# Optimization experiments

Measured on AMD Instinct MI355X. Metric: run time of the kernel, lower is better.

Reference implementation:

```python
import jax, jax.numpy as jnp
import numpy as np

DIM = 128
EPS = 1e-5

def _layernorm(x, w, b, eps=EPS):
    mu = jnp.mean(x, axis=-1, keepdims=True)
    var = jnp.mean(jnp.square(x - mu), axis=-1, keepdims=True)
    return (x - mu) * jax.lax.rsqrt(var + eps) * w + b

def setup_inputs() -> dict:
    key = jax.random.key(0)
    ks = jax.random.split(key, 6)
    B, N, D = 1, 512, DIM
    x = jax.random.normal(ks[0], (B, N, N, D), dtype=jnp.float32)
    mask = jnp.ones((B, N, N), dtype=jnp.float32)
    # parameters (torch Linear weight is [out, in]; we store [in, out] for x @ W)
    lecun = 1.0 / np.sqrt(D)
    w_p_in = jax.random.normal(ks[1], (D, 2 * D), dtype=jnp.float32) * lecun
    w_g_in = jnp.zeros((D, 2 * D), dtype=jnp.float32)   # gating_init -> zeros
    w_p_out = jnp.zeros((D, D), dtype=jnp.float32)      # final_init -> zeros
    w_g_out = jnp.zeros((D, D), dtype=jnp.float32)      # gating_init -> zeros
    # use small random values instead of exact zeros to make the math non-trivial
    w_g_in = jax.random.normal(ks[2], (D, 2 * D), dtype=jnp.float32) * 0.02
    w_p_out = jax.random.normal(ks[3], (D, D), dtype=jnp.float32) * 0.02
    w_g_out = jax.random.normal(ks[4], (D, D), dtype=jnp.float32) * 0.02
    norm_in_w = jnp.ones((D,), jnp.float32)
    norm_in_b = jnp.zeros((D,), jnp.float32)
    norm_out_w = jnp.ones((D,), jnp.float32)
    norm_out_b = jnp.zeros((D,), jnp.float32)
    return {
        "x": x, "mask": mask,
        "w_p_in": w_p_in, "w_g_in": w_g_in,
        "w_p_out": w_p_out, "w_g_out": w_g_out,
        "norm_in_w": norm_in_w, "norm_in_b": norm_in_b,
        "norm_out_w": norm_out_w, "norm_out_b": norm_out_b,
    }

def reference(x, mask, w_p_in, w_g_in, w_p_out, w_g_out,
              norm_in_w, norm_in_b, norm_out_w, norm_out_b):
    # x: [B,N,N,D], mask: [B,N,N]
    xn = _layernorm(x, norm_in_w, norm_in_b)          # norm_in
    x_in = xn
    p = xn @ w_p_in                                   # [B,N,N,2D]
    g = jax.nn.sigmoid(xn @ w_g_in)
    h = p * g * mask[..., None]                       # gated + masked
    a, b = jnp.split(h.astype(jnp.float32), 2, axis=-1)  # each [B,N,N,D]
    t = jnp.einsum('bikd,bjkd->bijd', a, b)           # triangular matmul
    tn = _layernorm(t, norm_out_w, norm_out_b)        # norm_out (eps=1e-5)
    out = (tn @ w_p_out) * jax.nn.sigmoid(x_in @ w_g_out)
    return out
```

## Files before the change

### kernel.cpp

```cpp
#include <hip/hip_runtime.h>
#include <hip/hip_bf16.h>
#include <math.h>

#define NN 512
#define DD 128
#define NP (NN*NN)

#define PITCH ((size_t)(NP * 2 + 256))

typedef __attribute__((ext_vector_type(4))) float f32x4;
typedef __attribute__((ext_vector_type(8))) short bf16x8;

__device__ __forceinline__ unsigned short f2bf(float f) {
  union { float f; unsigned u; } v; v.f = f;
  unsigned r = v.u + 0x7FFFu + ((v.u >> 16) & 1u);
  return (unsigned short)(r >> 16);
}
__device__ __forceinline__ float bf2f(unsigned short h) {
  union { unsigned u; float f; } v; v.u = ((unsigned)h) << 16;
  return v.f;
}
__device__ __forceinline__ float sigmoidf_(float x) {
  return __builtin_amdgcn_rcpf(1.0f + __expf(-x));
}
__device__ __forceinline__ unsigned pkbf2(float a, float b) {
  float2 t; t.x = a; t.y = b;
  __hip_bfloat162 h = __float22bfloat162_rn(t);
  unsigned r; __builtin_memcpy(&r, &h, 4); return r;
}

__device__ __forceinline__ void gll16(void* lds, const void* g) {
  __builtin_amdgcn_global_load_lds(
      (const __attribute__((address_space(1))) void*)g,
      (__attribute__((address_space(3))) void*)lds, 16, 0, 0);
}

#define WP_P  0
#define WP_G  65536
#define WP_GO 131072
#define WP_PO 163840

__global__ __launch_bounds__(256) void kw_prep(const float* __restrict__ w_p_in,
    const float* __restrict__ w_g_in, const float* __restrict__ w_g_out,
    const float* __restrict__ w_p_out, unsigned short* __restrict__ wprep) {
  int idx = blockIdx.x * 256 + threadIdx.x;
  int n, k, base; float v;
  if (idx < 32768)       { n = idx >> 7;          k = idx & 127; v = w_p_in[k * 256 + n];  base = WP_P; }
  else if (idx < 65536)  { int e = idx - 32768;  n = e >> 7; k = e & 127; v = w_g_in[k * 256 + n];  base = WP_G; }
  else if (idx < 81920)  { int e = idx - 65536;  n = e >> 7; k = e & 127; v = w_g_out[k * 128 + n]; base = WP_GO; }
  else                   { int e = idx - 81920;  n = e >> 7; k = e & 127; v = w_p_out[k * 128 + n]; base = WP_PO; }
  int dst = base + n * 256 + ((2 * k) ^ ((n & 7) << 4));
  wprep[dst >> 1] = f2bf(v);
}

__global__ __launch_bounds__(256) void kA_ln(const float* __restrict__ x,
    const float* __restrict__ nw, const float* __restrict__ nb,
    unsigned short* __restrict__ xn_sw) {
  const int tid = threadIdx.x;
  const int l16 = tid & 15, rsub = tid >> 4;
  const int row0 = blockIdx.x * 64;
  const float4 wv0 = *(const float4*)(nw + l16 * 8);
  const float4 wv1 = *(const float4*)(nw + l16 * 8 + 4);
  const float4 bv0 = *(const float4*)(nb + l16 * 8);
  const float4 bv1 = *(const float4*)(nb + l16 * 8 + 4);
  #pragma unroll
  for (int rnd = 0; rnd < 4; ++rnd) {
    int r = row0 + rnd * 16 + rsub;
    const float* xr = x + (size_t)r * DD + l16 * 8;
    float4 v0 = *(const float4*)xr;
    float4 v1 = *(const float4*)(xr + 4);
    float s = v0.x + v0.y + v0.z + v0.w + v1.x + v1.y + v1.z + v1.w;
    float q = v0.x*v0.x + v0.y*v0.y + v0.z*v0.z + v0.w*v0.w
            + v1.x*v1.x + v1.y*v1.y + v1.z*v1.z + v1.w*v1.w;
    #pragma unroll
    for (int m = 8; m; m >>= 1) { s += __shfl_xor(s, m); q += __shfl_xor(q, m); }
    float mean = s * (1.0f / DD);
    float var = q * (1.0f / DD) - mean * mean;
    float rstd = rsqrtf(var + 1e-5f);
    uint4 pk;
    pk.x = pkbf2((v0.x - mean) * rstd * wv0.x + bv0.x, (v0.y - mean) * rstd * wv0.y + bv0.y);
    pk.y = pkbf2((v0.z - mean) * rstd * wv0.z + bv0.z, (v0.w - mean) * rstd * wv0.w + bv0.w);
    pk.z = pkbf2((v1.x - mean) * rstd * wv1.x + bv1.x, (v1.y - mean) * rstd * wv1.y + bv1.y);
    pk.w = pkbf2((v1.z - mean) * rstd * wv1.z + bv1.z, (v1.w - mean) * rstd * wv1.w + bv1.w);
    *(uint4*)((unsigned char*)xn_sw + (size_t)r * 256 + ((l16 * 16) ^ ((r & 7) << 4))) = pk;
  }
}

__global__ __launch_bounds__(256) void kB_gemm(
    const unsigned short* __restrict__ xn_sw, const float* __restrict__ mask,
    const unsigned short* __restrict__ wprep,
    unsigned char* __restrict__ a_t, unsigned char* __restrict__ b_t) {
  const int q = blockIdx.x;
  const int row0 = blockIdx.y * 128;
  const int tid = threadIdx.x, lane = tid & 63, wv = tid >> 6;
  const int wr = wv >> 1, wc = wv & 1;
  __shared__ __align__(16) unsigned char sxn[32768];
  __shared__ __align__(16) unsigned char sepi[16384];
  __shared__ float smask[128];

  #pragma unroll
  for (int it = 0; it < 8; ++it) {
    int o = it * 4096 + tid * 16;
    gll16(sxn + o, (const unsigned char*)xn_sw + (size_t)row0 * 256 + o);
  }
  if (tid < 128) smask[tid] = mask[row0 + tid];
  __syncthreads();

  const unsigned char* wp = (const unsigned char*)wprep;

  f32x4 acc[4][4] = {};
  #pragma unroll
  for (int ks = 0; ks < 4; ++ks) {
    int kb = ks * 64 + (lane >> 4) * 16;
    bf16x8 af[4], bfr[4];
    #pragma unroll
    for (int mi = 0; mi < 4; ++mi) {
      int r = wr * 64 + mi * 16 + (lane & 15);
      af[mi] = *(const bf16x8*)(sxn + r * 256 + (kb ^ ((r & 7) << 4)));
    }
    #pragma unroll
    for (int ni = 0; ni < 2; ++ni) {
      int n = q * 64 + wc * 32 + ni * 16 + (lane & 15);
      int off = n * 256 + (kb ^ ((n & 7) << 4));
      bfr[ni]     = *(const bf16x8*)(wp + WP_P + off);
      bfr[ni + 2] = *(const bf16x8*)(wp + WP_G + off);
    }
    #pragma unroll
    for (int mi = 0; mi < 4; ++mi)
      #pragma unroll
      for (int ni = 0; ni < 4; ++ni)
        acc[mi][ni] = __builtin_amdgcn_mfma_f32_16x16x32_bf16(af[mi], bfr[ni], acc[mi][ni], 0, 0, 0);
  }

  #pragma unroll
  for (int mi = 0; mi < 4; ++mi) {
    int rq = wr * 64 + mi * 16 + (lane >> 4) * 4;
    float mk0 = smask[rq], mk1 = smask[rq + 1], mk2 = smask[rq + 2], mk3 = smask[rq + 3];
    #pragma unroll
    for (int ni = 0; ni < 2; ++ni) {
      int drel = wc * 32 + ni * 16 + (lane & 15);
      uint2 pk;
      pk.x = pkbf2(acc[mi][ni][0] * sigmoidf_(acc[mi][ni + 2][0]) * mk0,
                   acc[mi][ni][1] * sigmoidf_(acc[mi][ni + 2][1]) * mk1);
      pk.y = pkbf2(acc[mi][ni][2] * sigmoidf_(acc[mi][ni + 2][2]) * mk2,
                   acc[mi][ni][3] * sigmoidf_(acc[mi][ni + 2][3]) * mk3);
      *(uint2*)(sepi + drel * 256 + ((rq * 2) ^ ((drel & 7) << 4))) = pk;
    }
  }
  __syncthreads();
  unsigned char* dst = (q < 2) ? a_t : b_t;
  const int dmin = (q & 1) * 64;
  #pragma unroll
  for (int it = 0; it < 4; ++it) {
    int idx = it * 256 + tid;
    int dr = idx >> 4, ch = idx & 15;
    uint4 v = *(const uint4*)(sepi + dr * 256 + ((ch * 16) ^ ((dr & 7) << 4)));
    *(uint4*)(dst + (size_t)(dmin + dr) * PITCH + (size_t)(row0 + ch * 8) * 2) = v;
  }
}

__global__ __launch_bounds__(256) void k2_einsum(
    const unsigned char* __restrict__ a_t, const unsigned char* __restrict__ b_t,
    unsigned char* __restrict__ t_out) {
  int bid = blockIdx.x;
  int wg = (bid & 7) * 256 + (bid >> 3);
  int d = wg >> 4;
  int tile = wg & 15;
  int i0 = (tile >> 2) * 128, j0 = (tile & 3) * 128;
  const int tid = threadIdx.x, lane = tid & 63, wv = tid >> 6;
  const int wr = wv >> 1, wc = wv & 1;
  __shared__ __align__(16) unsigned char smem[32768];
  unsigned char* sA0 = smem;
  unsigned char* sB0 = smem + 16384;
  const unsigned char* Abase = a_t + (size_t)d * PITCH + (size_t)i0 * 1024;
  const unsigned char* Bbase = b_t + (size_t)d * PITCH + (size_t)j0 * 1024;

  const int so0 = tid * 16;
  const int r0s = so0 >> 6, c0s = (so0 >> 4) & 3;
  const size_t ga0 = (size_t)r0s * 1024 + ((c0s ^ ((r0s >> 1) & 3)) << 4);
  const int so1 = so0 + 4096;
  const int r1s = so1 >> 6, c1s = (so1 >> 4) & 3;
  const size_t ga1 = (size_t)r1s * 1024 + ((c1s ^ ((r1s >> 1) & 3)) << 4);

  f32x4 acc[4][4] = {};
  gll16(sA0 + so0, Abase + ga0);
  gll16(sB0 + so0, Bbase + ga0);
  gll16(sA0 + so1, Abase + ga1);
  gll16(sB0 + so1, Bbase + ga1);
  __syncthreads();

  int cur = 0;
  for (int t = 0; t < 16; ++t) {
    if (t < 15) {
      int nk = (t + 1) * 64;
      int nb_ = (cur ^ 1) * 8192;
      gll16(sA0 + nb_ + so0, Abase + ga0 + nk);
      gll16(sB0 + nb_ + so0, Bbase + ga0 + nk);
      gll16(sA0 + nb_ + so1, Abase + ga1 + nk);
      gll16(sB0 + nb_ + so1, Bbase + ga1 + nk);
    }
    bf16x8 af[4], bfr[4];
    const int kc = lane >> 4;
    int cb = cur * 8192;
    #pragma unroll
    for (int mi = 0; mi < 4; ++mi) {
      int r = wr * 64 + mi * 16 + (lane & 15);
      af[mi] = *(const bf16x8*)(sA0 + cb + r * 64 + ((kc ^ ((r >> 1) & 3)) << 4));
    }
    #pragma unroll
    for (int ni = 0; ni < 4; ++ni) {
      int r = wc * 64 + ni * 16 + (lane & 15);
      bfr[ni] = *(const bf16x8*)(sB0 + cb + r * 64 + ((kc ^ ((r >> 1) & 3)) << 4));
    }
    #pragma unroll
    for (int mi = 0; mi < 4; ++mi)
      #pragma unroll
      for (int ni = 0; ni < 4; ++ni)
        acc[mi][ni] = __builtin_amdgcn_mfma_f32_16x16x32_bf16(af[mi], bfr[ni], acc[mi][ni], 0, 0, 0);
    __syncthreads();
    cur ^= 1;
  }

  #pragma unroll
  for (int mi = 0; mi < 4; ++mi)
    #pragma unroll
    for (int j = 0; j < 4; ++j) {
      int il = wr * 64 + mi * 16 + (lane >> 4) * 4 + j;
      #pragma unroll
      for (int ni = 0; ni < 4; ++ni) {
        int jl = wc * 64 + ni * 16 + (lane & 15);
        *(unsigned short*)(smem + il * 256 + ((jl * 2) ^ ((il & 7) << 4))) = f2bf(acc[mi][ni][j]);
      }
    }
  __syncthreads();
  unsigned char* trow = t_out + (size_t)d * PITCH;
  #pragma unroll
  for (int rr = 0; rr < 8; ++rr) {
    int idx = rr * 256 + tid;
    int il = idx >> 4, ch = idx & 15;
    uint4 v = *(const uint4*)(smem + il * 256 + ((ch * 16) ^ ((il & 7) << 4)));
    *(uint4*)(trow + (size_t)(i0 + il) * 1024 + (size_t)(j0 + ch * 8) * 2) = v;
  }
}

__global__ __launch_bounds__(256) void k3_out(
    const unsigned char* __restrict__ t_in, const unsigned short* __restrict__ xn_sw,
    const unsigned short* __restrict__ wprep,
    const float* __restrict__ now, const float* __restrict__ nob,
    float* __restrict__ out) {
  const int p0 = blockIdx.x * 64;
  const int tid = threadIdx.x, lane = tid & 63, wv = tid >> 6;
  const int wr = wv >> 1, wc = wv & 1;
  __shared__ __align__(16) unsigned short sT[128 * 64];
  __shared__ __align__(16) unsigned char sTN[64 * 256];
  __shared__ __align__(16) unsigned char sxn[64 * 256];
  __shared__ float ps[4][64], pq[4][64], smean[64], srstd[64];

  #pragma unroll
  for (int it = 0; it < 4; ++it) {
    int o = it * 4096 + tid * 16;
    int dr = o >> 7, cb = o & 127;
    gll16((unsigned char*)sT + o, t_in + (size_t)dr * PITCH + (size_t)p0 * 2 + cb);
  }
  #pragma unroll
  for (int it = 0; it < 4; ++it) {
    int o = it * 4096 + tid * 16;
    gll16(sxn + o, (const unsigned char*)xn_sw + (size_t)p0 * 256 + o);
  }
  __syncthreads();
  const int p = tid & 63, dh = tid >> 6;
  {
    float s = 0.f, q = 0.f;
    #pragma unroll
    for (int dd = 0; dd < 32; ++dd) {
      float v = bf2f(sT[(dh * 32 + dd) * 64 + p]);
      s += v; q += v * v;
    }
    ps[dh][p] = s; pq[dh][p] = q;
  }
  __syncthreads();
  if (tid < 64) {
    float s = ps[0][tid] + ps[1][tid] + ps[2][tid] + ps[3][tid];
    float q = pq[0][tid] + pq[1][tid] + pq[2][tid] + pq[3][tid];
    float mean = s * (1.0f / 128.0f);
    float var = q * (1.0f / 128.0f) - mean * mean;
    smean[tid] = mean; srstd[tid] = rsqrtf(var + 1e-5f);
  }
  __syncthreads();
  {
    float mean = smean[p], rstd = srstd[p];
    #pragma unroll
    for (int e = 0; e < 16; ++e) {
      int d0 = dh * 32 + e * 2;
      float v0 = (bf2f(sT[d0 * 64 + p]) - mean) * rstd * now[d0] + nob[d0];
      float v1 = (bf2f(sT[(d0 + 1) * 64 + p]) - mean) * rstd * now[d0 + 1] + nob[d0 + 1];
      unsigned pack = pkbf2(v0, v1);
      *(unsigned*)(sTN + p * 256 + ((d0 * 2) ^ ((p & 7) << 4))) = pack;
    }
  }
  __syncthreads();
  f32x4 accP[2][4] = {}, accG[2][4] = {};
  const unsigned char* wpo = (const unsigned char*)wprep + WP_PO;
  const unsigned char* wgo = (const unsigned char*)wprep + WP_GO;
  #pragma unroll
  for (int ks = 0; ks < 4; ++ks) {
    int kb = ks * 64 + (lane >> 4) * 16;
    bf16x8 af[2], ag[2], bP[4], bG[4];
    #pragma unroll
    for (int mi = 0; mi < 2; ++mi) {
      int r = wr * 32 + mi * 16 + (lane & 15);
      int off = r * 256 + (kb ^ ((r & 7) << 4));
      af[mi] = *(const bf16x8*)(sTN + off);
      ag[mi] = *(const bf16x8*)(sxn + off);
    }
    #pragma unroll
    for (int ni = 0; ni < 4; ++ni) {
      int n = wc * 64 + ni * 16 + (lane & 15);
      int off = n * 256 + (kb ^ ((n & 7) << 4));
      bP[ni] = *(const bf16x8*)(wpo + off);
      bG[ni] = *(const bf16x8*)(wgo + off);
    }
    #pragma unroll
    for (int mi = 0; mi < 2; ++mi)
      #pragma unroll
      for (int ni = 0; ni < 4; ++ni) {
        accP[mi][ni] = __builtin_amdgcn_mfma_f32_16x16x32_bf16(af[mi], bP[ni], accP[mi][ni], 0, 0, 0);
        accG[mi][ni] = __builtin_amdgcn_mfma_f32_16x16x32_bf16(ag[mi], bG[ni], accG[mi][ni], 0, 0, 0);
      }
  }
  #pragma unroll
  for (int mi = 0; mi < 2; ++mi)
    #pragma unroll
    for (int ni = 0; ni < 4; ++ni) {
      int n = wc * 64 + ni * 16 + (lane & 15);
      int prow = wr * 32 + mi * 16 + (lane >> 4) * 4;
      #pragma unroll
      for (int j = 0; j < 4; ++j)
        out[(size_t)(p0 + prow + j) * 128 + n] = accP[mi][ni][j] * sigmoidf_(accG[mi][ni][j]);
    }
}

extern "C" void kernel_launch(void* const* d_in, const int* in_sizes, int n_in,
                              void* d_out, int out_size, void* d_ws, size_t ws_size,
                              hipStream_t stream) {
  (void)in_sizes; (void)n_in; (void)out_size; (void)ws_size;
  const float* x         = (const float*)d_in[0];
  const float* mask      = (const float*)d_in[1];
  const float* w_p_in    = (const float*)d_in[2];
  const float* w_g_in    = (const float*)d_in[3];
  const float* w_p_out   = (const float*)d_in[4];
  const float* w_g_out   = (const float*)d_in[5];
  const float* norm_in_w = (const float*)d_in[6];
  const float* norm_in_b = (const float*)d_in[7];
  const float* norm_out_w= (const float*)d_in[8];
  const float* norm_out_b= (const float*)d_in[9];
  float* out = (float*)d_out;

  unsigned char* ws = (unsigned char*)d_ws;
  const size_t SLAB = (size_t)128 * PITCH;
  unsigned char* a_t    = ws;
  unsigned char* b_t    = ws + SLAB;
  unsigned char* t_buf  = ws + 2 * SLAB;
  unsigned short* xn_sw = (unsigned short*)(ws + 3 * SLAB);
  unsigned short* wprep = (unsigned short*)(ws + 3 * SLAB + (size_t)NP * 256);

  kw_prep<<<384, 256, 0, stream>>>(w_p_in, w_g_in, w_g_out, w_p_out, wprep);
  kA_ln<<<4096, 256, 0, stream>>>(x, norm_in_w, norm_in_b, xn_sw);
  dim3 gb(4, 2048);
  kB_gemm<<<gb, 256, 0, stream>>>(xn_sw, mask, wprep, a_t, b_t);
  k2_einsum<<<2048, 256, 0, stream>>>(a_t, b_t, t_buf);
  k3_out<<<4096, 256, 0, stream>>>(t_buf, xn_sw, wprep, norm_out_w, norm_out_b, out);
}
```

Measured before the change: 252.0 us.

## Fuse input layernorm into projection GEMM and stage output stores through LDS

Merges the layernorm kernel and the input projection GEMM into one kernel. Each block normalizes 128 rows into shared memory and then loops over all four output column quarters. This removes a launch and the four-fold re-read of xn from global memory, at the cost of fewer, longer blocks. It also changes the output kernel to write its results through a swizzled LDS buffer so the global stores become coalesced 16-byte writes instead of scattered 4-byte ones.

New measurement: 246.6 us. 1.02x faster.

```diff
diff --git a/kernel.cpp b/kernel.cpp
--- a/kernel.cpp
+++ b/kernel.cpp
@@ -53,20 +53,29 @@
   wprep[dst >> 1] = f2bf(v);
 }
 
-__global__ __launch_bounds__(256) void kA_ln(const float* __restrict__ x,
+__global__ __launch_bounds__(256) void kAB(
+    const float* __restrict__ x, const float* __restrict__ mask,
+    const unsigned short* __restrict__ wprep,
     const float* __restrict__ nw, const float* __restrict__ nb,
-    unsigned short* __restrict__ xn_sw) {
-  const int tid = threadIdx.x;
+    unsigned short* __restrict__ xn_sw,
+    unsigned char* __restrict__ a_t, unsigned char* __restrict__ b_t) {
+  const int row0 = blockIdx.x * 128;
+  const int tid = threadIdx.x, lane = tid & 63, wv = tid >> 6;
+  const int wr = wv >> 1, wc = wv & 1;
+  __shared__ __align__(16) unsigned char sxn[32768];
+  __shared__ __align__(16) unsigned char sepi[16384];
+  __shared__ float smask[128];
+
   const int l16 = tid & 15, rsub = tid >> 4;
-  const int row0 = blockIdx.x * 64;
+  if (tid < 128) smask[tid] = mask[row0 + tid];
   const float4 wv0 = *(const float4*)(nw + l16 * 8);
   const float4 wv1 = *(const float4*)(nw + l16 * 8 + 4);
   const float4 bv0 = *(const float4*)(nb + l16 * 8);
   const float4 bv1 = *(const float4*)(nb + l16 * 8 + 4);
   #pragma unroll
-  for (int rnd = 0; rnd < 4; ++rnd) {
-    int r = row0 + rnd * 16 + rsub;
-    const float* xr = x + (size_t)r * DD + l16 * 8;
+  for (int rnd = 0; rnd < 8; ++rnd) {
+    int r = rnd * 16 + rsub;
+    const float* xr = x + (size_t)(row0 + r) * DD + l16 * 8;
     float4 v0 = *(const float4*)xr;
     float4 v1 = *(const float4*)(xr + 4);
     float s = v0.x + v0.y + v0.z + v0.w + v1.x + v1.y + v1.z + v1.w;
@@ -82,80 +91,64 @@
     pk.y = pkbf2((v0.z - mean) * rstd * wv0.z + bv0.z, (v0.w - mean) * rstd * wv0.w + bv0.w);
     pk.z = pkbf2((v1.x - mean) * rstd * wv1.x + bv1.x, (v1.y - mean) * rstd * wv1.y + bv1.y);
     pk.w = pkbf2((v1.z - mean) * rstd * wv1.z + bv1.z, (v1.w - mean) * rstd * wv1.w + bv1.w);
-    *(uint4*)((unsigned char*)xn_sw + (size_t)r * 256 + ((l16 * 16) ^ ((r & 7) << 4))) = pk;
-  }
-}
-
-__global__ __launch_bounds__(256) void kB_gemm(
-    const unsigned short* __restrict__ xn_sw, const float* __restrict__ mask,
-    const unsigned short* __restrict__ wprep,
-    unsigned char* __restrict__ a_t, unsigned char* __restrict__ b_t) {
-  const int q = blockIdx.x;
-  const int row0 = blockIdx.y * 128;
-  const int tid = threadIdx.x, lane = tid & 63, wv = tid >> 6;
-  const int wr = wv >> 1, wc = wv & 1;
-  __shared__ __align__(16) unsigned char sxn[32768];
-  __shared__ __align__(16) unsigned char sepi[16384];
-  __shared__ float smask[128];
-
-  #pragma unroll
-  for (int it = 0; it < 8; ++it) {
-    int o = it * 4096 + tid * 16;
-    gll16(sxn + o, (const unsigned char*)xn_sw + (size_t)row0 * 256 + o);
-  }
-  if (tid < 128) smask[tid] = mask[row0 + tid];
+    int off = ((l16 * 16) ^ ((r & 7) << 4));
+    *(uint4*)(sxn + r * 256 + off) = pk;
+    *(uint4*)((unsigned char*)xn_sw + (size_t)(row0 + r) * 256 + off) = pk;
+  }
   __syncthreads();
 
   const unsigned char* wp = (const unsigned char*)wprep;
 
-  f32x4 acc[4][4] = {};
-  #pragma unroll
-  for (int ks = 0; ks < 4; ++ks) {
-    int kb = ks * 64 + (lane >> 4) * 16;
-    bf16x8 af[4], bfr[4];
+  for (int q = 0; q < 4; ++q) {
+    f32x4 acc[4][4] = {};
+    #pragma unroll
+    for (int ks = 0; ks < 4; ++ks) {
+      int kb = ks * 64 + (lane >> 4) * 16;
+      bf16x8 af[4], bfr[4];
+      #pragma unroll
+      for (int mi = 0; mi < 4; ++mi) {
+        int r = wr * 64 + mi * 16 + (lane & 15);
+        af[mi] = *(const bf16x8*)(sxn + r * 256 + (kb ^ ((r & 7) << 4)));
+      }
+      #pragma unroll
+      for (int ni = 0; ni < 2; ++ni) {
+        int n = q * 64 + wc * 32 + ni * 16 + (lane & 15);
+        int off = n * 256 + (kb ^ ((n & 7) << 4));
+        bfr[ni]     = *(const bf16x8*)(wp + WP_P + off);
+        bfr[ni + 2] = *(const bf16x8*)(wp + WP_G + off);
+      }
+      #pragma unroll
+      for (int mi = 0; mi < 4; ++mi)
+        #pragma unroll
+        for (int ni = 0; ni < 4; ++ni)
+          acc[mi][ni] = __builtin_amdgcn_mfma_f32_16x16x32_bf16(af[mi], bfr[ni], acc[mi][ni], 0, 0, 0);
+    }
     #pragma unroll
     for (int mi = 0; mi < 4; ++mi) {
-      int r = wr * 64 + mi * 16 + (lane & 15);
-      af[mi] = *(const bf16x8*)(sxn + r * 256 + (kb ^ ((r & 7) << 4)));
-    }
-    #pragma unroll
-    for (int ni = 0; ni < 2; ++ni) {
-      int n = q * 64 + wc * 32 + ni * 16 + (lane & 15);
-      int off = n * 256 + (kb ^ ((n & 7) << 4));
-      bfr[ni]     = *(const bf16x8*)(wp + WP_P + off);
-      bfr[ni + 2] = *(const bf16x8*)(wp + WP_G + off);
-    }
-    #pragma unroll
-    for (int mi = 0; mi < 4; ++mi)
-      #pragma unroll
-      for (int ni = 0; ni < 4; ++ni)
-        acc[mi][ni] = __builtin_amdgcn_mfma_f32_16x16x32_bf16(af[mi], bfr[ni], acc[mi][ni], 0, 0, 0);
-  }
-
-  #pragma unroll
-  for (int mi = 0; mi < 4; ++mi) {
-    int rq = wr * 64 + mi * 16 + (lane >> 4) * 4;
-    float mk0 = smask[rq], mk1 = smask[rq + 1], mk2 = smask[rq + 2], mk3 = smask[rq + 3];
-    #pragma unroll
-    for (int ni = 0; ni < 2; ++ni) {
-      int drel = wc * 32 + ni * 16 + (lane & 15);
-      uint2 pk;
-      pk.x = pkbf2(acc[mi][ni][0] * sigmoidf_(acc[mi][ni + 2][0]) * mk0,
-                   acc[mi][ni][1] * sigmoidf_(acc[mi][ni + 2][1]) * mk1);
-      pk.y = pkbf2(acc[mi][ni][2] * sigmoidf_(acc[mi][ni + 2][2]) * mk2,
-                   acc[mi][ni][3] * sigmoidf_(acc[mi][ni + 2][3]) * mk3);
-      *(uint2*)(sepi + drel * 256 + ((rq * 2) ^ ((drel & 7) << 4))) = pk;
-    }
-  }
-  __syncthreads();
-  unsigned char* dst = (q < 2) ? a_t : b_t;
-  const int dmin = (q & 1) * 64;
-  #pragma unroll
-  for (int it = 0; it < 4; ++it) {
-    int idx = it * 256 + tid;
-    int dr = idx >> 4, ch = idx & 15;
-    uint4 v = *(const uint4*)(sepi + dr * 256 + ((ch * 16) ^ ((dr & 7) << 4)));
-    *(uint4*)(dst + (size_t)(dmin + dr) * PITCH + (size_t)(row0 + ch * 8) * 2) = v;
+      int rq = wr * 64 + mi * 16 + (lane >> 4) * 4;
+      float mk0 = smask[rq], mk1 = smask[rq + 1], mk2 = smask[rq + 2], mk3 = smask[rq + 3];
+      #pragma unroll
+      for (int ni = 0; ni < 2; ++ni) {
+        int drel = wc * 32 + ni * 16 + (lane & 15);
+        uint2 pk;
+        pk.x = pkbf2(acc[mi][ni][0] * sigmoidf_(acc[mi][ni + 2][0]) * mk0,
+                     acc[mi][ni][1] * sigmoidf_(acc[mi][ni + 2][1]) * mk1);
+        pk.y = pkbf2(acc[mi][ni][2] * sigmoidf_(acc[mi][ni + 2][2]) * mk2,
+                     acc[mi][ni][3] * sigmoidf_(acc[mi][ni + 2][3]) * mk3);
+        *(uint2*)(sepi + drel * 256 + ((rq * 2) ^ ((drel & 7) << 4))) = pk;
+      }
+    }
+    __syncthreads();
+    unsigned char* dst = (q < 2) ? a_t : b_t;
+    const int dmin = (q & 1) * 64;
+    #pragma unroll
+    for (int it = 0; it < 4; ++it) {
+      int idx = it * 256 + tid;
+      int dr = idx >> 4, ch = idx & 15;
+      uint4 v = *(const uint4*)(sepi + dr * 256 + ((ch * 16) ^ ((dr & 7) << 4)));
+      *(uint4*)(dst + (size_t)(dmin + dr) * PITCH + (size_t)(row0 + ch * 8) * 2) = v;
+    }
+    __syncthreads();
   }
 }
 
@@ -251,9 +244,10 @@
   const int p0 = blockIdx.x * 64;
   const int tid = threadIdx.x, lane = tid & 63, wv = tid >> 6;
   const int wr = wv >> 1, wc = wv & 1;
-  __shared__ __align__(16) unsigned short sT[128 * 64];
-  __shared__ __align__(16) unsigned char sTN[64 * 256];
-  __shared__ __align__(16) unsigned char sxn[64 * 256];
+  __shared__ __align__(16) unsigned char sm[49152];
+  unsigned short* sT = (unsigned short*)sm;
+  unsigned char* sTN = sm + 16384;
+  unsigned char* sxn = sm + 32768;
   __shared__ float ps[4][64], pq[4][64], smean[64], srstd[64];
 
   #pragma unroll
@@ -328,16 +322,28 @@
         accG[mi][ni] = __builtin_amdgcn_mfma_f32_16x16x32_bf16(ag[mi], bG[ni], accG[mi][ni], 0, 0, 0);
       }
   }
+  __syncthreads();
   #pragma unroll
   for (int mi = 0; mi < 2; ++mi)
     #pragma unroll
     for (int ni = 0; ni < 4; ++ni) {
-      int n = wc * 64 + ni * 16 + (lane & 15);
+      int nb4 = (wc * 256 + ni * 64 + (lane & 15) * 4);
       int prow = wr * 32 + mi * 16 + (lane >> 4) * 4;
       #pragma unroll
-      for (int j = 0; j < 4; ++j)
-        out[(size_t)(p0 + prow + j) * 128 + n] = accP[mi][ni][j] * sigmoidf_(accG[mi][ni][j]);
-    }
+      for (int j = 0; j < 4; ++j) {
+        int pp = prow + j;
+        float v = accP[mi][ni][j] * sigmoidf_(accG[mi][ni][j]);
+        *(float*)(sm + pp * 512 + (nb4 ^ (((pp >> 2) & 3) << 6))) = v;
+      }
+    }
+  __syncthreads();
+  #pragma unroll
+  for (int it = 0; it < 8; ++it) {
+    int idx = it * 256 + tid;
+    int pp = idx >> 5, ch = idx & 31;
+    uint4 v = *(const uint4*)(sm + pp * 512 + ((ch * 16) ^ (((pp >> 2) & 3) << 6)));
+    *(uint4*)((unsigned char*)out + (size_t)(p0 + pp) * 512 + ch * 16) = v;
+  }
 }
 
 extern "C" void kernel_launch(void* const* d_in, const int* in_sizes, int n_in,
@@ -365,9 +371,7 @@
   unsigned short* wprep = (unsigned short*)(ws + 3 * SLAB + (size_t)NP * 256);
 
   kw_prep<<<384, 256, 0, stream>>>(w_p_in, w_g_in, w_g_out, w_p_out, wprep);
-  kA_ln<<<4096, 256, 0, stream>>>(x, norm_in_w, norm_in_b, xn_sw);
-  dim3 gb(4, 2048);
-  kB_gemm<<<gb, 256, 0, stream>>>(xn_sw, mask, wprep, a_t, b_t);
+  kAB<<<2048, 256, 0, stream>>>(x, mask, wprep, norm_in_w, norm_in_b, xn_sw, a_t, b_t);
   k2_einsum<<<2048, 256, 0, stream>>>(a_t, b_t, t_buf);
   k3_out<<<4096, 256, 0, stream>>>(t_buf, xn_sw, wprep, norm_out_w, norm_out_b, out);
 }
```
